# Kernel optimization log

Measured on AMD Instinct MI355X. Metric: run time of the kernel, lower is better.

## Reference

```python
import jax, jax.numpy as jnp
import numpy as np

N = 50000      # nodes
E = 800000     # edges
T_MAX = 128
N_T = 128
NF = T_MAX * 3 # 384 node features


def setup_inputs() -> dict:
    key = jax.random.key(0)
    ks = jax.random.split(key, 12)
    def lin(k, fi, fo):
        k1, k2 = jax.random.split(k)
        s = 1.0 / np.sqrt(fi)
        return (jax.random.uniform(k1, (fi, fo), jnp.float32, -s, s),
                jax.random.uniform(k2, (fo,), jnp.float32, -s, s))
    x = jax.random.normal(ks[0], (N, NF), jnp.float32)
    edge_index = jax.random.randint(ks[1], (2, E), 0, N, jnp.int32)
    W1, b1 = lin(ks[2], NF, N_T)
    W2, b2 = lin(ks[3], N_T, N_T * 3)
    W3, b3 = lin(ks[4], N_T * 3, N_T * 2)
    W4, b4 = lin(ks[5], N_T * 2, NF)
    Wl, bl = lin(ks[6], NF, T_MAX)
    return {"x": x, "edge_index": edge_index,
            "W1": W1, "b1": b1, "W2": W2, "b2": b2,
            "W3": W3, "b3": b3, "W4": W4, "b4": b4,
            "Wl": Wl, "bl": bl}


def reference(x, edge_index, W1, b1, W2, b2, W3, b3, W4, b4, Wl, bl):
    # GCNConv (PyG defaults): add self-loops, symmetric normalization
    loop = jnp.arange(N, dtype=edge_index.dtype)
    src = jnp.concatenate([edge_index[0], loop])
    dst = jnp.concatenate([edge_index[1], loop])
    deg = jax.ops.segment_sum(jnp.ones_like(src, jnp.float32), dst, num_segments=N)
    dinv = jax.lax.rsqrt(deg)  # deg >= 1 due to self-loops
    norm = (dinv[src] * dinv[dst])[:, None]  # [E+N, 1]

    def gcn(h, W, b):
        hw = h @ W                       # [N, out]
        msg = hw[src] * norm             # gather + scale per edge
        agg = jax.ops.segment_sum(msg, dst, num_segments=N)
        return agg + b

    # dropout is identity in eval mode
    h = jax.nn.leaky_relu(gcn(x, W1, b1))
    h = jax.nn.leaky_relu(gcn(h, W2, b2))
    h = jax.nn.leaky_relu(gcn(h, W3, b3))
    h = jax.nn.leaky_relu(gcn(h, W4, b4))
    h = h @ Wl + bl
    return jax.nn.relu(h)  # args.schedule_deviation == False
```

## Files before the change

### kernel.cpp

```cpp
#include <hip/hip_runtime.h>

#define NNODES 50000
#define NEDGES 800000
#define NTILES ((NNODES + 255) / 256)
#define XFEAT (NNODES * 384)
#define XPREP_BLOCKS (XFEAT / (256 * 8))
#define WPREP_TOTAL 344064
#define WPREP_BLOCKS (WPREP_TOTAL / 256)
#define NODES_PER_SLICE (NNODES / 8)
#define EDGES_PER_BLOCK 2048
#define EDGE_BLOCKS ((NEDGES + EDGES_PER_BLOCK - 1) / EDGES_PER_BLOCK)

typedef unsigned short ushort_t;
typedef __attribute__((ext_vector_type(8))) short short8;
typedef __attribute__((ext_vector_type(4))) float floatx4;

__device__ __forceinline__ float bf2f(unsigned short u) {
  union { unsigned int i; float f; } v; v.i = ((unsigned int)u) << 16; return v.f;
}
__device__ __forceinline__ unsigned short f2bf(float f) {
  union { float f; unsigned int i; } v; v.f = f;
  unsigned int r = v.i + 0x7fffu + ((v.i >> 16) & 1u);
  return (unsigned short)(r >> 16);
}

__device__ __forceinline__ void gload_lds16(const void* g, void* l) {
  __builtin_amdgcn_global_load_lds(
      (const __attribute__((address_space(1))) unsigned int*)g,
      (__attribute__((address_space(3))) unsigned int*)l, 16, 0, 0);
}

template <int N>
__device__ __forceinline__ void wait_vmcnt() {
  if constexpr (N == 0)      asm volatile("s_waitcnt vmcnt(0)" ::: "memory");
  else if constexpr (N == 3) asm volatile("s_waitcnt vmcnt(3)" ::: "memory");
  else if constexpr (N == 6) asm volatile("s_waitcnt vmcnt(6)" ::: "memory");
  else                       asm volatile("s_waitcnt vmcnt(0)" ::: "memory");
}


__global__ __launch_bounds__(256) void hist_kernel(const int* __restrict__ dst,
                                                   int* __restrict__ cnt) {
  int b = blockIdx.x;
  int lo = (b & 7) * NODES_PER_SLICE, hi = lo + NODES_PER_SLICE;
  int base = (b >> 3) * EDGES_PER_BLOCK + threadIdx.x;
#pragma unroll
  for (int q = 0; q < EDGES_PER_BLOCK / 256; ++q) {
    int i = base + q * 256;
    if (i < NEDGES) {
      int d = dst[i];
      if (d >= lo && d < hi) atomicAdd(&cnt[d], 1);
    }
  }
}

__global__ __launch_bounds__(256) void fill_kernel(const int* __restrict__ src,
                                                   const int* __restrict__ dst,
                                                   int* __restrict__ cursor,
                                                   int* __restrict__ col_idx) {
  int b = blockIdx.x;
  int lo = (b & 7) * NODES_PER_SLICE, hi = lo + NODES_PER_SLICE;
  int base = (b >> 3) * EDGES_PER_BLOCK + threadIdx.x;
#pragma unroll
  for (int q = 0; q < EDGES_PER_BLOCK / 256; ++q) {
    int i = base + q * 256;
    if (i < NEDGES) {
      int d = dst[i];
      int s = src[i];
      if (d >= lo && d < hi) {
        int p = atomicAdd(&cursor[d], 1);
        col_idx[p] = s;
      }
    }
  }
}


__global__ __launch_bounds__(256) void tile_scan_kernel(
    const int* __restrict__ cnt, int* __restrict__ tile_pref, int* __restrict__ tile_sum) {
  __shared__ int s[256];
  int b = blockIdx.x, t = threadIdx.x;
  int i = b * 256 + t;
  int v = (i < NNODES) ? cnt[i] : 0;
  s[t] = v;
  __syncthreads();
#pragma unroll
  for (int off = 1; off < 256; off <<= 1) {
    int x = (t >= off) ? s[t - off] : 0;
    __syncthreads();
    s[t] += x;
    __syncthreads();
  }
  if (i < NNODES) tile_pref[i] = s[t] - v;
  if (t == 255) tile_sum[b] = s[255];
}

__global__ __launch_bounds__(256) void sum_scan_kernel(
    const int* __restrict__ tile_sum, int* __restrict__ tile_base) {
  __shared__ int s[256];
  int t = threadIdx.x;
  int v = (t < NTILES) ? tile_sum[t] : 0;
  s[t] = v;
  __syncthreads();
#pragma unroll
  for (int off = 1; off < 256; off <<= 1) {
    int x = (t >= off) ? s[t - off] : 0;
    __syncthreads();
    s[t] += x;
    __syncthreads();
  }
  if (t < NTILES) tile_base[t] = s[t] - v;
}

__global__ __launch_bounds__(256) void scan_write_kernel(
    const int* __restrict__ cnt, const int* __restrict__ tile_pref,
    const int* __restrict__ tile_base, int* __restrict__ row_ptr,
    int* __restrict__ cursor, float* __restrict__ dinv) {
  int b = blockIdx.x, t = threadIdx.x;
  int i = b * 256 + t;
  if (i < NNODES) {
    int base = tile_base[b] + tile_pref[i];
    row_ptr[i] = base;
    cursor[i] = base;
    dinv[i] = rsqrtf((float)(cnt[i] + 1));
    if (i == NNODES - 1) row_ptr[NNODES] = base + cnt[i];
  }
}

__global__ __launch_bounds__(256) void prep_all(
    const float* __restrict__ x, ushort_t* __restrict__ xbf,
    const float* __restrict__ W1, ushort_t* __restrict__ W1h, ushort_t* __restrict__ W1l,
    const float* __restrict__ W2, ushort_t* __restrict__ W2h, ushort_t* __restrict__ W2l,
    const float* __restrict__ W3, ushort_t* __restrict__ W3h, ushort_t* __restrict__ W3l,
    const float* __restrict__ W4, ushort_t* __restrict__ W4h, ushort_t* __restrict__ W4l,
    const float* __restrict__ Wl, ushort_t* __restrict__ Wlh, ushort_t* __restrict__ Wll) {
  int b = blockIdx.x;
  if (b < XPREP_BLOCKS) {
    size_t i = ((size_t)b * 256 + threadIdx.x) * 8;
    float4 p0 = *(const float4*)(x + i);
    float4 p1 = *(const float4*)(x + i + 4);
    uint4 u;
    u.x = (unsigned int)f2bf(p0.x) | ((unsigned int)f2bf(p0.y) << 16);
    u.y = (unsigned int)f2bf(p0.z) | ((unsigned int)f2bf(p0.w) << 16);
    u.z = (unsigned int)f2bf(p1.x) | ((unsigned int)f2bf(p1.y) << 16);
    u.w = (unsigned int)f2bf(p1.z) | ((unsigned int)f2bf(p1.w) << 16);
    *(uint4*)(xbf + i) = u;
    return;
  }
  int t = (b - XPREP_BLOCKS) * 256 + threadIdx.x;
  const float* W; ushort_t* hi; ushort_t* lo; int K, N;
  if (t < 49152)       { W = W1; hi = W1h; lo = W1l; K = 384; N = 128; }
  else if (t < 98304)  { W = W2; hi = W2h; lo = W2l; K = 128; N = 384; t -= 49152; }
  else if (t < 196608) { W = W3; hi = W3h; lo = W3l; K = 384; N = 256; t -= 98304; }
  else if (t < 294912) { W = W4; hi = W4h; lo = W4l; K = 256; N = 384; t -= 196608; }
  else                 { W = Wl; hi = Wlh; lo = Wll; K = 384; N = 128; t -= 294912; }
  int n = t / K, k = t - n * K;
  float w = W[(size_t)k * N + n];
  unsigned short h = f2bf(w);
  hi[t] = h;
  lo[t] = f2bf(w - bf2f(h));
}


template <int WH>
__device__ __forceinline__ void load_rowh(const ushort_t* p, float* f) {
  if (WH == 1) {
    f[0] = bf2f(*p);
  } else {
    unsigned int u = *(const unsigned int*)p;
    f[0] = bf2f((unsigned short)(u & 0xffff));
    f[1] = bf2f((unsigned short)(u >> 16));
  }
}

template <int C>
__global__ __launch_bounds__(256) void agg_kernel(
    const ushort_t* __restrict__ in, ushort_t* __restrict__ out,
    const int* __restrict__ row_ptr, const int* __restrict__ col_idx,
    const float* __restrict__ dinv, const float* __restrict__ bias,
    int mode, int scale_store) {
  constexpr int WH = C / 128;
  int b = blockIdx.x;
  int half = (b >> 2) & 1;
  int idx = (b >> 3) * 4 + (b & 3);
  if (idx >= 3125) return;
  int wave = idx * 4 + (int)(threadIdx.x >> 6);
  int lane = threadIdx.x & 63;
  int co = half * (C / 2) + lane * WH;
  const ushort_t* base = in + co;
  float bb[WH];
  if (mode) {
    if (WH == 1) {
      bb[0] = bias[co];
    } else {
      float2 b2 = *(const float2*)(bias + co);
      bb[0] = b2.x; bb[1] = b2.y;
    }
  }
  for (int k = 0; k < 4; ++k) {
    int wid = __builtin_amdgcn_readfirstlane(wave * 4 + k);
    float acc[WH];
    load_rowh<WH>(base + (size_t)wid * C, acc);
    int e = row_ptr[wid], e1 = row_ptr[wid + 1];
    for (; e + 16 <= e1; e += 16) {
      int j[16];
#pragma unroll
      for (int q = 0; q < 16; ++q) j[q] = col_idx[e + q];
      float v[16][WH];
#pragma unroll
      for (int q = 0; q < 16; ++q) load_rowh<WH>(base + (size_t)j[q] * C, v[q]);
#pragma unroll
      for (int c = 0; c < WH; ++c) {
        float s0 = (v[0][c] + v[1][c]) + (v[2][c] + v[3][c]);
        float s1 = (v[4][c] + v[5][c]) + (v[6][c] + v[7][c]);
        float s2 = (v[8][c] + v[9][c]) + (v[10][c] + v[11][c]);
        float s3 = (v[12][c] + v[13][c]) + (v[14][c] + v[15][c]);
        acc[c] += (s0 + s1) + (s2 + s3);
      }
    }
    for (; e + 4 <= e1; e += 4) {
      int j0 = col_idx[e], j1 = col_idx[e + 1], j2 = col_idx[e + 2], j3 = col_idx[e + 3];
      float v0[WH], v1[WH], v2[WH], v3[WH];
      load_rowh<WH>(base + (size_t)j0 * C, v0);
      load_rowh<WH>(base + (size_t)j1 * C, v1);
      load_rowh<WH>(base + (size_t)j2 * C, v2);
      load_rowh<WH>(base + (size_t)j3 * C, v3);
#pragma unroll
      for (int c = 0; c < WH; ++c) acc[c] += (v0[c] + v1[c]) + (v2[c] + v3[c]);
    }
    for (; e < e1; ++e) {
      int j = col_idx[e];
      float v[WH];
      load_rowh<WH>(base + (size_t)j * C, v);
#pragma unroll
      for (int c = 0; c < WH; ++c) acc[c] += v[c];
    }
    float di = dinv[wid];
    if (mode) {
      float sc = scale_store ? di : 1.f;
#pragma unroll
      for (int c = 0; c < WH; ++c) {
        float v = acc[c] * di + bb[c];
        v = v > 0.f ? v : 0.01f * v;
        acc[c] = v * sc;
      }
    } else {
#pragma unroll
      for (int c = 0; c < WH; ++c) acc[c] *= di;
    }
    if (WH == 1) {
      out[(size_t)wid * C + co] = f2bf(acc[0]);
    } else {
      *(unsigned int*)(out + (size_t)wid * C + co) =
          (unsigned int)f2bf(acc[0]) | ((unsigned int)f2bf(acc[1]) << 16);
    }
  }
}


#define BK 32

template <int TB>
__device__ __forceinline__ void stage_tile(const ushort_t* __restrict__ G, int g0,
                                           int K, int kb, ushort_t* lds,
                                           int tid, int w, int Mclamp) {
  constexpr int IT = TB / 64;
#pragma unroll
  for (int it = 0; it < IT; ++it) {
    int s = it * 256 + tid;
    int row = s >> 2;
    int j = (s & 3) ^ ((s >> 3) & 3);
    int gr = g0 + row; if (gr > Mclamp - 1) gr = Mclamp - 1;
    gload_lds16(G + (size_t)gr * K + kb + j * 8,
                lds + (size_t)(it * 256 + w * 64) * 8);
  }
}

template <int TBM, int TBN>
__global__ __launch_bounds__(256, TBM == 64 ? 6 : 3) void gemm_mfma(
    const ushort_t* __restrict__ A, const ushort_t* __restrict__ Bhi,
    const ushort_t* __restrict__ Blo, void* __restrict__ Cv,
    const float* __restrict__ bias, const float* __restrict__ dinv,
    int M, int K, int ldc, int mode, int scale_store, int out_f32) {
  constexpr int FR = TBM / 32;
  constexpr int FG = TBN / 32;
  constexpr int NLD = TBM / 64 + 2 * (TBN / 64);
  __shared__ ushort_t As[2][TBM * BK];
  __shared__ ushort_t Bh[2][TBN * BK];
  __shared__ ushort_t Bl[2][TBN * BK];
  int tid = threadIdx.x;
  int lane = tid & 63, w = tid >> 6;
  int wm = w & 1, wn = w >> 1;

  int lin = blockIdx.y * gridDim.x + blockIdx.x;
  int nwg = gridDim.x * gridDim.y;
  int q = nwg >> 3, r = nwg & 7, xc = lin & 7, sdx = lin >> 3;
  int wg = (xc < r ? xc * (q + 1) : r * (q + 1) + (xc - r) * q) + sdx;
  int nty = gridDim.y;
  int tx = wg / nty, ty = wg - tx * nty;
  int m0 = tx * TBM, n0 = ty * TBN;

  floatx4 acc[FR][FG] = {};
  int nkt = K / BK;
  int cur = 0;
  stage_tile<TBM>(A, m0, K, 0, As[0], tid, w, M);
  stage_tile<TBN>(Bhi, n0, K, 0, Bh[0], tid, w, 1 << 30);
  stage_tile<TBN>(Blo, n0, K, 0, Bl[0], tid, w, 1 << 30);
  int rr = lane & 15, jj = lane >> 4;
  for (int kt = 0; kt < nkt; ++kt) {
    if (kt + 1 < nkt) {
      int kb = (kt + 1) * BK;
      stage_tile<TBM>(A, m0, K, kb, As[cur ^ 1], tid, w, M);
      stage_tile<TBN>(Bhi, n0, K, kb, Bh[cur ^ 1], tid, w, 1 << 30);
      stage_tile<TBN>(Blo, n0, K, kb, Bl[cur ^ 1], tid, w, 1 << 30);
      wait_vmcnt<NLD>();
    } else {
      wait_vmcnt<0>();
    }
    __builtin_amdgcn_s_barrier();
    __builtin_amdgcn_sched_barrier(0);
    short8 af[FR], fh[FG], fl[FG];
#pragma unroll
    for (int f = 0; f < FR; ++f) {
      int fr_row = wm * (TBM / 2) + f * 16 + rr;
      af[f] = *(const short8*)&As[cur][fr_row * BK + ((jj ^ ((fr_row >> 1) & 3)) * 8)];
    }
#pragma unroll
    for (int g = 0; g < FG; ++g) {
      int fb_row = wn * (TBN / 2) + g * 16 + rr;
      int o = fb_row * BK + ((jj ^ ((fb_row >> 1) & 3)) * 8);
      fh[g] = *(const short8*)&Bh[cur][o];
      fl[g] = *(const short8*)&Bl[cur][o];
    }
#pragma unroll
    for (int f = 0; f < FR; ++f)
#pragma unroll
      for (int g = 0; g < FG; ++g) {
        acc[f][g] = __builtin_amdgcn_mfma_f32_16x16x32_bf16(af[f], fh[g], acc[f][g], 0, 0, 0);
        acc[f][g] = __builtin_amdgcn_mfma_f32_16x16x32_bf16(af[f], fl[g], acc[f][g], 0, 0, 0);
      }
    __builtin_amdgcn_sched_barrier(0);
    __builtin_amdgcn_s_barrier();
    cur ^= 1;
  }
  int cr = lane >> 4, cc = lane & 15;
#pragma unroll
  for (int f = 0; f < FR; ++f) {
#pragma unroll
    for (int r2 = 0; r2 < 4; ++r2) {
      int row = m0 + wm * (TBM / 2) + f * 16 + cr * 4 + r2;
      if (row >= M) continue;
      float sc = scale_store ? dinv[row] : 1.f;
#pragma unroll
      for (int g = 0; g < FG; ++g) {
        int col = n0 + wn * (TBN / 2) + g * 16 + cc;
        float v = acc[f][g][r2];
        if (mode) {
          v += bias[col];
          v = (mode == 1) ? (v > 0.f ? v : 0.01f * v) : (v > 0.f ? v : 0.f);
        }
        v *= sc;
        if (out_f32) ((float*)Cv)[(size_t)row * ldc + col] = v;
        else ((ushort_t*)Cv)[(size_t)row * ldc + col] = f2bf(v);
      }
    }
  }
}


extern "C" void kernel_launch(void* const* d_in, const int* in_sizes, int n_in,
                              void* d_out, int out_size, void* d_ws, size_t ws_size,
                              hipStream_t stream) {
  const float* x  = (const float*)d_in[0];
  const int* ei   = (const int*)d_in[1];
  const float* W1 = (const float*)d_in[2];
  const float* b1 = (const float*)d_in[3];
  const float* W2 = (const float*)d_in[4];
  const float* b2 = (const float*)d_in[5];
  const float* W3 = (const float*)d_in[6];
  const float* b3 = (const float*)d_in[7];
  const float* W4 = (const float*)d_in[8];
  const float* b4 = (const float*)d_in[9];
  const float* Wl = (const float*)d_in[10];
  const float* bl = (const float*)d_in[11];

  char* p = (char*)d_ws;
  auto alloc = [&](size_t bytes) {
    char* r = p;
    p += (bytes + 255) & ~(size_t)255;
    return r;
  };
  int* cnt       = (int*)alloc((size_t)NNODES * 4);
  int* cursor    = (int*)alloc((size_t)NNODES * 4);
  int* row_ptr   = (int*)alloc((size_t)(NNODES + 1) * 4);
  float* dinv    = (float*)alloc((size_t)NNODES * 4);
  int* col_idx   = (int*)alloc((size_t)NEDGES * 4);
  int* tile_pref = (int*)alloc((size_t)NNODES * 4);
  int* tile_sum  = (int*)alloc(256 * 4);
  int* tile_base = (int*)alloc(256 * 4);
  ushort_t* W1h = (ushort_t*)alloc(49152 * 2); ushort_t* W1l = (ushort_t*)alloc(49152 * 2);
  ushort_t* W2h = (ushort_t*)alloc(49152 * 2); ushort_t* W2l = (ushort_t*)alloc(49152 * 2);
  ushort_t* W3h = (ushort_t*)alloc(98304 * 2); ushort_t* W3l = (ushort_t*)alloc(98304 * 2);
  ushort_t* W4h = (ushort_t*)alloc(98304 * 2); ushort_t* W4l = (ushort_t*)alloc(98304 * 2);
  ushort_t* Wlh = (ushort_t*)alloc(49152 * 2); ushort_t* Wll = (ushort_t*)alloc(49152 * 2);
  ushort_t* actA = (ushort_t*)alloc((size_t)NNODES * 384 * 2);
  ushort_t* actB = (ushort_t*)alloc((size_t)NNODES * 384 * 2);
  ushort_t* xbf = actB;

  const int* src = ei;
  const int* dst = ei + NEDGES;

  hipMemsetAsync(cnt, 0, (size_t)NNODES * 4, stream);
  hist_kernel<<<EDGE_BLOCKS * 8, 256, 0, stream>>>(dst, cnt);
  tile_scan_kernel<<<NTILES, 256, 0, stream>>>(cnt, tile_pref, tile_sum);
  sum_scan_kernel<<<1, 256, 0, stream>>>(tile_sum, tile_base);
  scan_write_kernel<<<NTILES, 256, 0, stream>>>(cnt, tile_pref, tile_base, row_ptr, cursor, dinv);
  fill_kernel<<<EDGE_BLOCKS * 8, 256, 0, stream>>>(src, dst, cursor, col_idx);

  prep_all<<<XPREP_BLOCKS + WPREP_BLOCKS, 256, 0, stream>>>(
      x, xbf, W1, W1h, W1l, W2, W2h, W2l, W3, W3h, W3l, W4, W4h, W4l, Wl, Wlh, Wll);

  dim3 blk(256);
  int gm64  = (NNODES + 63) / 64;
  int gm128 = (NNODES + 127) / 128;
  int gagg  = 6256;

  gemm_mfma<64, 64><<<dim3(gm64, 2), blk, 0, stream>>>(xbf, W1h, W1l, actA, (const float*)0, dinv, NNODES, 384, 128, 0, 1, 0);
  agg_kernel<128><<<gagg, blk, 0, stream>>>(actA, actB, row_ptr, col_idx, dinv, b1, 1, 1);
  agg_kernel<128><<<gagg, blk, 0, stream>>>(actB, actA, row_ptr, col_idx, dinv, (const float*)0, 0, 0);
  gemm_mfma<128, 128><<<dim3(gm128, 3), blk, 0, stream>>>(actA, W2h, W2l, actB, b2, dinv, NNODES, 128, 384, 1, 0, 0);
  gemm_mfma<128, 128><<<dim3(gm128, 2), blk, 0, stream>>>(actB, W3h, W3l, actA, (const float*)0, dinv, NNODES, 384, 256, 0, 1, 0);
  agg_kernel<256><<<gagg, blk, 0, stream>>>(actA, actB, row_ptr, col_idx, dinv, b3, 1, 1);
  agg_kernel<256><<<gagg, blk, 0, stream>>>(actB, actA, row_ptr, col_idx, dinv, (const float*)0, 0, 0);
  gemm_mfma<128, 128><<<dim3(gm128, 3), blk, 0, stream>>>(actA, W4h, W4l, actB, b4, dinv, NNODES, 256, 384, 1, 0, 0);
  gemm_mfma<64, 64><<<dim3(gm64, 2), blk, 0, stream>>>(actB, Wlh, Wll, d_out, bl, dinv, NNODES, 384, 128, 2, 0, 1);
}
```

Before: 588.0 us.

## Remap aggregation so each wave handles four nodes over 64-byte column slices

```diff
diff --git a/kernel.cpp b/kernel.cpp
--- a/kernel.cpp
+++ b/kernel.cpp
@@ -162,99 +162,62 @@
 }
 
 
-template <int WH>
-__device__ __forceinline__ void load_rowh(const ushort_t* p, float* f) {
-  if (WH == 1) {
-    f[0] = bf2f(*p);
-  } else {
-    unsigned int u = *(const unsigned int*)p;
-    f[0] = bf2f((unsigned short)(u & 0xffff));
-    f[1] = bf2f((unsigned short)(u >> 16));
-  }
-}
-
 template <int C>
 __global__ __launch_bounds__(256) void agg_kernel(
     const ushort_t* __restrict__ in, ushort_t* __restrict__ out,
     const int* __restrict__ row_ptr, const int* __restrict__ col_idx,
     const float* __restrict__ dinv, const float* __restrict__ bias,
     int mode, int scale_store) {
-  constexpr int WH = C / 128;
+  constexpr int NSL = (C * 2) / 64;
   int b = blockIdx.x;
-  int half = (b >> 2) & 1;
-  int idx = (b >> 3) * 4 + (b & 3);
-  if (idx >= 3125) return;
-  int wave = idx * 4 + (int)(threadIdx.x >> 6);
+  int role = b & 7;
+  int slice = role & (NSL - 1);
+  int nbase = (NSL == 8) ? 0 : (role >> 2) * (NNODES / 2);
+  int nn = (NSL == 8) ? NNODES : (NNODES / 2);
+  int idx = b >> 3;
   int lane = threadIdx.x & 63;
-  int co = half * (C / 2) + lane * WH;
-  const ushort_t* base = in + co;
-  float bb[WH];
+  int wv = threadIdx.x >> 6;
+  int g = lane >> 4, sub = lane & 15;
+  int node = nbase + idx * 16 + wv * 4 + g;
+  if (node >= nbase + nn) return;
+  int co = slice * 32 + sub * 2;
+  const ushort_t* basep = in + co;
+  int e = row_ptr[node], e1 = row_ptr[node + 1];
+  float acc0, acc1;
+  {
+    unsigned int u = *(const unsigned int*)(basep + (size_t)node * C);
+    acc0 = bf2f((unsigned short)(u & 0xffff));
+    acc1 = bf2f((unsigned short)(u >> 16));
+  }
+  for (; e + 4 <= e1; e += 4) {
+    int j0 = col_idx[e], j1 = col_idx[e + 1], j2 = col_idx[e + 2], j3 = col_idx[e + 3];
+    unsigned int u0 = *(const unsigned int*)(basep + (size_t)j0 * C);
+    unsigned int u1 = *(const unsigned int*)(basep + (size_t)j1 * C);
+    unsigned int u2 = *(const unsigned int*)(basep + (size_t)j2 * C);
+    unsigned int u3 = *(const unsigned int*)(basep + (size_t)j3 * C);
+    acc0 += (bf2f((unsigned short)(u0 & 0xffff)) + bf2f((unsigned short)(u1 & 0xffff))) +
+            (bf2f((unsigned short)(u2 & 0xffff)) + bf2f((unsigned short)(u3 & 0xffff)));
+    acc1 += (bf2f((unsigned short)(u0 >> 16)) + bf2f((unsigned short)(u1 >> 16))) +
+            (bf2f((unsigned short)(u2 >> 16)) + bf2f((unsigned short)(u3 >> 16)));
+  }
+  for (; e < e1; ++e) {
+    int j = col_idx[e];
+    unsigned int u = *(const unsigned int*)(basep + (size_t)j * C);
+    acc0 += bf2f((unsigned short)(u & 0xffff));
+    acc1 += bf2f((unsigned short)(u >> 16));
+  }
+  float di = dinv[node];
   if (mode) {
-    if (WH == 1) {
-      bb[0] = bias[co];
-    } else {
-      float2 b2 = *(const float2*)(bias + co);
-      bb[0] = b2.x; bb[1] = b2.y;
-    }
-  }
-  for (int k = 0; k < 4; ++k) {
-    int wid = __builtin_amdgcn_readfirstlane(wave * 4 + k);
-    float acc[WH];
-    load_rowh<WH>(base + (size_t)wid * C, acc);
-    int e = row_ptr[wid], e1 = row_ptr[wid + 1];
-    for (; e + 16 <= e1; e += 16) {
-      int j[16];
-#pragma unroll
-      for (int q = 0; q < 16; ++q) j[q] = col_idx[e + q];
-      float v[16][WH];
-#pragma unroll
-      for (int q = 0; q < 16; ++q) load_rowh<WH>(base + (size_t)j[q] * C, v[q]);
-#pragma unroll
-      for (int c = 0; c < WH; ++c) {
-        float s0 = (v[0][c] + v[1][c]) + (v[2][c] + v[3][c]);
-        float s1 = (v[4][c] + v[5][c]) + (v[6][c] + v[7][c]);
-        float s2 = (v[8][c] + v[9][c]) + (v[10][c] + v[11][c]);
-        float s3 = (v[12][c] + v[13][c]) + (v[14][c] + v[15][c]);
-        acc[c] += (s0 + s1) + (s2 + s3);
-      }
-    }
-    for (; e + 4 <= e1; e += 4) {
-      int j0 = col_idx[e], j1 = col_idx[e + 1], j2 = col_idx[e + 2], j3 = col_idx[e + 3];
-      float v0[WH], v1[WH], v2[WH], v3[WH];
-      load_rowh<WH>(base + (size_t)j0 * C, v0);
-      load_rowh<WH>(base + (size_t)j1 * C, v1);
-      load_rowh<WH>(base + (size_t)j2 * C, v2);
-      load_rowh<WH>(base + (size_t)j3 * C, v3);
-#pragma unroll
-      for (int c = 0; c < WH; ++c) acc[c] += (v0[c] + v1[c]) + (v2[c] + v3[c]);
-    }
-    for (; e < e1; ++e) {
-      int j = col_idx[e];
-      float v[WH];
-      load_rowh<WH>(base + (size_t)j * C, v);
-#pragma unroll
-      for (int c = 0; c < WH; ++c) acc[c] += v[c];
-    }
-    float di = dinv[wid];
-    if (mode) {
-      float sc = scale_store ? di : 1.f;
-#pragma unroll
-      for (int c = 0; c < WH; ++c) {
-        float v = acc[c] * di + bb[c];
-        v = v > 0.f ? v : 0.01f * v;
-        acc[c] = v * sc;
-      }
-    } else {
-#pragma unroll
-      for (int c = 0; c < WH; ++c) acc[c] *= di;
-    }
-    if (WH == 1) {
-      out[(size_t)wid * C + co] = f2bf(acc[0]);
-    } else {
-      *(unsigned int*)(out + (size_t)wid * C + co) =
-          (unsigned int)f2bf(acc[0]) | ((unsigned int)f2bf(acc[1]) << 16);
-    }
-  }
+    float2 b2 = *(const float2*)(bias + co);
+    float sc = scale_store ? di : 1.f;
+    float x0 = acc0 * di + b2.x; x0 = x0 > 0.f ? x0 : 0.01f * x0;
+    float x1 = acc1 * di + b2.y; x1 = x1 > 0.f ? x1 : 0.01f * x1;
+    acc0 = x0 * sc; acc1 = x1 * sc;
+  } else {
+    acc0 *= di; acc1 *= di;
+  }
+  *(unsigned int*)(out + (size_t)node * C + co) =
+      (unsigned int)f2bf(acc0) | ((unsigned int)f2bf(acc1) << 16);
 }
 
 
@@ -423,15 +386,16 @@
   dim3 blk(256);
   int gm64  = (NNODES + 63) / 64;
   int gm128 = (NNODES + 127) / 128;
-  int gagg  = 6256;
+  int gagg128 = 8 * 1563;
+  int gagg256 = 8 * 3125;
 
   gemm_mfma<64, 64><<<dim3(gm64, 2), blk, 0, stream>>>(xbf, W1h, W1l, actA, (const float*)0, dinv, NNODES, 384, 128, 0, 1, 0);
-  agg_kernel<128><<<gagg, blk, 0, stream>>>(actA, actB, row_ptr, col_idx, dinv, b1, 1, 1);
-  agg_kernel<128><<<gagg, blk, 0, stream>>>(actB, actA, row_ptr, col_idx, dinv, (const float*)0, 0, 0);
+  agg_kernel<128><<<gagg128, blk, 0, stream>>>(actA, actB, row_ptr, col_idx, dinv, b1, 1, 1);
+  agg_kernel<128><<<gagg128, blk, 0, stream>>>(actB, actA, row_ptr, col_idx, dinv, (const float*)0, 0, 0);
   gemm_mfma<128, 128><<<dim3(gm128, 3), blk, 0, stream>>>(actA, W2h, W2l, actB, b2, dinv, NNODES, 128, 384, 1, 0, 0);
   gemm_mfma<128, 128><<<dim3(gm128, 2), blk, 0, stream>>>(actB, W3h, W3l, actA, (const float*)0, dinv, NNODES, 384, 256, 0, 1, 0);
-  agg_kernel<256><<<gagg, blk, 0, stream>>>(actA, actB, row_ptr, col_idx, dinv, b3, 1, 1);
-  agg_kernel<256><<<gagg, blk, 0, stream>>>(actB, actA, row_ptr, col_idx, dinv, (const float*)0, 0, 0);
+  agg_kernel<256><<<gagg256, blk, 0, stream>>>(actA, actB, row_ptr, col_idx, dinv, b3, 1, 1);
+  agg_kernel<256><<<gagg256, blk, 0, stream>>>(actB, actA, row_ptr, col_idx, dinv, (const float*)0, 0, 0);
   gemm_mfma<128, 128><<<dim3(gm128, 3), blk, 0, stream>>>(actA, W4h, W4l, actB, b4, dinv, NNODES, 256, 384, 1, 0, 0);
   gemm_mfma<64, 64><<<dim3(gm64, 2), blk, 0, stream>>>(actB, Wlh, Wll, d_out, bl, dinv, NNODES, 384, 128, 2, 0, 1);
 }
```

Measured after the change: 684.4 us. 16.4% more time.
